# Kernel tuning notes

Hardware: AMD Instinct MI355X
Metric: run time of the kernel (lower is better)

Reference implementation:

```python
import jax, jax.numpy as jnp
import numpy as np

TAU_FILTER_INV = 1000.0
DT = 0.001
# decay = 1 - alpha = exp(-dt * tau_filter_inv)
DECAY = float(np.exp(-DT * TAU_FILTER_INV))


def setup_inputs() -> dict:
    key = jax.random.key(0)
    k1, k2, k3 = jax.random.split(key, 3)
    T, B, I, O = 2048, 32, 256, 256
    input_tensor = jax.random.normal(k1, (T, B, I), dtype=jnp.float32)
    # Linear weight init mimics uniform(-k, k), k = sqrt(1/input_size)
    k = float(np.sqrt(1.0 / I))
    W = jax.random.uniform(k2, (O, I), dtype=jnp.float32, minval=-k, maxval=k)
    b = jax.random.uniform(k3, (O,), dtype=jnp.float32, minval=-k, maxval=k)
    return {"input_tensor": input_tensor, "W": W, "b": b}


def reference(input_tensor, W, b):
    # Dense projection: [T, B, I] @ [I, O] -> [T, B, O]
    y = jnp.einsum("tbi,oi->tbo", input_tensor, W) + b
    decay = jnp.asarray(DECAY, dtype=y.dtype)

    # s(t) = y(t) + decay * s(t-1); s(0) = y(0) (init state 0)
    def step(s, x):
        s = x + decay * s
        return s, s

    _, out = jax.lax.scan(step, jnp.zeros_like(y[0]), y)
    return out
```

## Files before the change

kernel.cpp:

```cpp
#include <hip/hip_runtime.h>
#include <cstddef>


#define DECAY  0.36787944117144233f
#define D9     1.2340980408667956e-4f
#define INV1MD 1.5819767068693265f

typedef __attribute__((ext_vector_type(8))) short short8;
typedef __attribute__((ext_vector_type(4))) short short4v;
typedef __attribute__((ext_vector_type(4))) float f32x4;

static constexpr int T_DIM = 2048, B_DIM = 32, K_DIM = 256, N_DIM = 256;
static constexpr int M_DIM = T_DIM * B_DIM;
static constexpr int PS  = 32768;
static constexpr int TCH = 64;

__device__ __forceinline__ float bfbits2f(unsigned short u) {
  unsigned int x = ((unsigned int)u) << 16;
  return __builtin_bit_cast(float, x);
}
__device__ __forceinline__ short f2bf_s(float f) {
  __bf16 h = (__bf16)f;
  return __builtin_bit_cast(short, h);
}

__global__ void k_split_w(const float* __restrict__ W, short* __restrict__ Wh) {
  const int o = blockIdx.x, i = threadIdx.x;
  size_t off = (size_t)(o >> 7) * PS + (i >> 5) * 4096 + ((i >> 3) & 3) * 1024 +
               (o & 127) * 8 + (i & 7);
  Wh[off] = f2bf_s(W[o * 256 + i]);
}

__global__ __launch_bounds__(512, 6)
void k_fused(const float* __restrict__ X, const short* __restrict__ Wth,
             const float* __restrict__ bias, float* __restrict__ out) {
  __shared__ __align__(16) char ldsA[32768];
  __shared__ __align__(16) short cbh[8 * 256];
  __shared__ float cfac[TCH];

  const int tid  = threadIdx.x;
  const int lane = tid & 63;
  const int wv   = tid >> 6;
  const int c    = blockIdx.x;
  const int b    = blockIdx.y;
  const int t0   = c * TCH;
  const int ch4  = lane * 4;

  const int row16 = lane & 15;
  const int kq    = lane >> 4;
  const int cg    = wv;
  const short* Wp = Wth + (size_t)(cg >> 2) * PS;
  const int wbase = kq * 1024 + ((cg & 3) * 32 + row16) * 8;

  if (tid < TCH)
    cfac[tid] = (1.f - __expf(-(float)(t0 + tid + 1))) * INV1MD;

  f32x4 y[9];
  {
    const int ts = t0 + wv * 9 - 8;
    if (ts >= 0) {
      const float* xp = X + (size_t)ts * 8192 + b * 256 + ch4;
      #pragma unroll
      for (int j = 0; j < 9; ++j)
        y[j] = *reinterpret_cast<const f32x4*>(xp + (size_t)j * 8192);
      f32x4 s = {0.f, 0.f, 0.f, 0.f};
      #pragma unroll
      for (int j = 0; j < 9; ++j) {
        #pragma unroll
        for (int e = 0; e < 4; ++e) s[e] = fmaf(DECAY, s[e], y[j][e]);
        y[j] = s;
      }
    } else {
      y[8] = *reinterpret_cast<const f32x4*>(X + b * 256 + ch4);
    }
  }
  {
    short4v cv;
    #pragma unroll
    for (int e = 0; e < 4; ++e) cv[e] = f2bf_s(y[8][e]);
    *reinterpret_cast<short4v*>(&cbh[wv * 256 + ch4]) = cv;
  }

  short8 bh[2][2];
  #pragma unroll
  for (int ct = 0; ct < 2; ++ct)
    bh[0][ct] = *reinterpret_cast<const short8*>(Wp + wbase + ct * 128);
  __builtin_amdgcn_sched_barrier(0);

  __syncthreads();

  f32x4 cin = {0.f, 0.f, 0.f, 0.f};
  {
    float m = 1.f;
    for (int v = wv - 1; v >= 0; --v) {
      short4v cv = *reinterpret_cast<const short4v*>(&cbh[v * 256 + ch4]);
      #pragma unroll
      for (int e = 0; e < 4; ++e)
        cin[e] = fmaf(bfbits2f((unsigned short)cv[e]), m, cin[e]);
      m *= D9;
    }
  }

  {
    static constexpr float DP[9] = {
        0.36787944117144233f, 0.1353352832366127f,  0.049787068367863944f,
        0.018315638888734179f, 0.006737946999085467f, 0.0024787521766663585f,
        0.0009118819655545162f, 0.00033546262790251185f, 1.2340980408667956e-4f};
    #pragma unroll
    for (int j = 0; j < 9; ++j) {
      const int r = wv * 9 + j - 8;
      if (r >= 0) {
        short4v hv;
        #pragma unroll
        for (int e = 0; e < 4; ++e)
          hv[e] = f2bf_s(fmaf(cin[e], DP[j], y[j][e]));
        const int byte = (r * 512 + ch4 * 2) ^ ((r & 7) << 4);
        *reinterpret_cast<short4v*>(ldsA + byte) = hv;
      }
    }
  }
  __syncthreads();

  f32x4 acc[4][2] = {};
  #pragma unroll
  for (int kt = 0; kt < 8; ++kt) {
    const int cur = kt & 1;
    if (kt < 7) {
      #pragma unroll
      for (int ct = 0; ct < 2; ++ct)
        bh[cur ^ 1][ct] = *reinterpret_cast<const short8*>(
            Wp + (kt + 1) * 4096 + wbase + ct * 128);
      __builtin_amdgcn_sched_barrier(0);
    }
    #pragma unroll
    for (int rh = 0; rh < 2; ++rh) {
      short8 ah0, ah1;
      {
        const int row0 = rh * 32 + row16;
        const int b0 = (row0 * 512 + kt * 64 + kq * 16) ^ ((row0 & 7) << 4);
        const int row1 = row0 + 16;
        const int b1 = (row1 * 512 + kt * 64 + kq * 16) ^ ((row1 & 7) << 4);
        ah0 = *reinterpret_cast<const short8*>(ldsA + b0);
        ah1 = *reinterpret_cast<const short8*>(ldsA + b1);
      }
      #pragma unroll
      for (int ct = 0; ct < 2; ++ct) {
        acc[rh * 2][ct] = __builtin_amdgcn_mfma_f32_16x16x32_bf16(
            ah0, bh[cur][ct], acc[rh * 2][ct], 0, 0, 0);
        acc[rh * 2 + 1][ct] = __builtin_amdgcn_mfma_f32_16x16x32_bf16(
            ah1, bh[cur][ct], acc[rh * 2 + 1][ct], 0, 0, 0);
      }
    }
  }

  const f32x4* bias4 = reinterpret_cast<const f32x4*>(bias);
  #pragma unroll
  for (int p = 0; p < 2; ++p) {
    __syncthreads();
    #pragma unroll
    for (int rt = 2 * p; rt < 2 * p + 2; ++rt)
      #pragma unroll
      for (int ct = 0; ct < 2; ++ct)
        #pragma unroll
        for (int j = 0; j < 4; ++j) {
          const int rowh = (rt * 16 + kq * 4 + j) & 31;
          const int col  = cg * 32 + ct * 16 + row16;
          const int byte = (rowh * 1024 + col * 4) ^ ((rowh & 7) << 4);
          *reinterpret_cast<float*>(ldsA + byte) = acc[rt][ct][j];
        }
    __syncthreads();
    #pragma unroll
    for (int q = 0; q < 4; ++q) {
      const int idx  = tid + q * 512;
      const int rowh = idx >> 6;
      const int colc = idx & 63;
      const int byte = (idx * 16) ^ ((rowh & 7) << 4);
      f32x4 yv = *reinterpret_cast<const f32x4*>(ldsA + byte);
      const int row = p * 32 + rowh;
      f32x4 bv = bias4[colc];
      const float cf = cfac[row];
      f32x4 r;
      #pragma unroll
      for (int e = 0; e < 4; ++e) r[e] = fmaf(bv[e], cf, yv[e]);
      __builtin_nontemporal_store(
          r, reinterpret_cast<f32x4*>(out + ((size_t)(t0 + row) * 32 + b) * 256 +
                                      colc * 4));
    }
  }
}

__global__ void k_fb_gemm(const float* __restrict__ X, const float* __restrict__ W,
                          const float* __restrict__ bias, float* __restrict__ Y) {
  size_t idx = (size_t)blockIdx.x * 256 + threadIdx.x;
  int o = (int)(idx & 255);
  size_t m = idx >> 8;
  const float* x = X + m * 256;
  const float* w = W + (size_t)o * 256;
  float s = bias[o];
  for (int k = 0; k < 256; ++k) s = fmaf(x[k], w[k], s);
  Y[idx] = s;
}
__global__ void k_fb_scan(float* __restrict__ Y) {
  int ch = blockIdx.x * 256 + threadIdx.x;
  float s = 0.f;
  float* p = Y + ch;
  for (int t = 0; t < 2048; ++t) { s = fmaf(DECAY, s, *p); *p = s; p += 8192; }
}

extern "C" void kernel_launch(void* const* d_in, const int* in_sizes, int n_in,
                              void* d_out, int out_size, void* d_ws, size_t ws_size,
                              hipStream_t stream) {
  const float* X    = (const float*)d_in[0];
  const float* W    = (const float*)d_in[1];
  const float* bias = (const float*)d_in[2];
  float* out = (float*)d_out;

  const size_t w_elems = (size_t)N_DIM * K_DIM;
  const size_t need    = w_elems * sizeof(short);

  if (ws_size >= need) {
    short* Wh = (short*)d_ws;
    k_split_w<<<N_DIM, 256, 0, stream>>>(W, Wh);
    k_fused<<<dim3(T_DIM / TCH, B_DIM), 512, 0, stream>>>(X, Wh, bias, out);
  } else {
    k_fb_gemm<<<M_DIM, 256, 0, stream>>>(X, W, bias, out);
    k_fb_scan<<<32, 256, 0, stream>>>(out);
  }
}
```

Baseline: 34.76 us.

## Process two time chunks per block, prefetching second chunk's inputs during first GEMM

Each block now handles two consecutive 64-step time chunks instead of one, halving the grid. The X loads for the second chunk are issued before the first chunk's MFMA/epilogue phase so their latency overlaps the compute. The launch-bounds occupancy hint drops from 6 to 4 blocks per CU, which frees registers for the extra prefetched state. The cost is half as many blocks to spread over the CUs and a longer serial path inside each block.

```diff
diff --git a/kernel.cpp b/kernel.cpp
--- a/kernel.cpp
+++ b/kernel.cpp
@@ -31,7 +31,7 @@
   Wh[off] = f2bf_s(W[o * 256 + i]);
 }
 
-__global__ __launch_bounds__(512, 6)
+__global__ __launch_bounds__(512, 4)
 void k_fused(const float* __restrict__ X, const short* __restrict__ Wth,
              const float* __restrict__ bias, float* __restrict__ out) {
   __shared__ __align__(16) char ldsA[32768];
@@ -41,9 +41,9 @@
   const int tid  = threadIdx.x;
   const int lane = tid & 63;
   const int wv   = tid >> 6;
-  const int c    = blockIdx.x;
+  const int c2   = blockIdx.x;
   const int b    = blockIdx.y;
-  const int t0   = c * TCH;
+  const int t0   = c2 * 2 * TCH;
   const int ch4  = lane * 4;
 
   const int row16 = lane & 15;
@@ -52,8 +52,110 @@
   const short* Wp = Wth + (size_t)(cg >> 2) * PS;
   const int wbase = kq * 1024 + ((cg & 3) * 32 + row16) * 8;
 
-  if (tid < TCH)
-    cfac[tid] = (1.f - __expf(-(float)(t0 + tid + 1))) * INV1MD;
+  static constexpr float DP[9] = {
+      0.36787944117144233f, 0.1353352832366127f,  0.049787068367863944f,
+      0.018315638888734179f, 0.006737946999085467f, 0.0024787521766663585f,
+      0.0009118819655545162f, 0.00033546262790251185f, 1.2340980408667956e-4f};
+
+  auto publish = [&](const f32x4& s) {
+    short4v cv;
+    #pragma unroll
+    for (int e = 0; e < 4; ++e) cv[e] = f2bf_s(s[e]);
+    *reinterpret_cast<short4v*>(&cbh[wv * 256 + ch4]) = cv;
+  };
+  auto combine = [&]() {
+    f32x4 cin = {0.f, 0.f, 0.f, 0.f};
+    float m = 1.f;
+    for (int v = wv - 1; v >= 0; --v) {
+      short4v cv = *reinterpret_cast<const short4v*>(&cbh[v * 256 + ch4]);
+      #pragma unroll
+      for (int e = 0; e < 4; ++e)
+        cin[e] = fmaf(bfbits2f((unsigned short)cv[e]), m, cin[e]);
+      m *= D9;
+    }
+    return cin;
+  };
+  auto fixup = [&](f32x4 (&y)[9], const f32x4& cin) {
+    #pragma unroll
+    for (int j = 0; j < 9; ++j) {
+      const int r = wv * 9 + j - 8;
+      if (r >= 0) {
+        short4v hv;
+        #pragma unroll
+        for (int e = 0; e < 4; ++e)
+          hv[e] = f2bf_s(fmaf(cin[e], DP[j], y[j][e]));
+        const int byte = (r * 512 + ch4 * 2) ^ ((r & 7) << 4);
+        *reinterpret_cast<short4v*>(ldsA + byte) = hv;
+      }
+    }
+  };
+  auto phase_be = [&](int t0c, short8 (&bh)[2][2]) {
+    f32x4 acc[4][2] = {};
+    #pragma unroll
+    for (int kt = 0; kt < 8; ++kt) {
+      const int cur = kt & 1;
+      if (kt < 7) {
+        #pragma unroll
+        for (int ct = 0; ct < 2; ++ct)
+          bh[cur ^ 1][ct] = *reinterpret_cast<const short8*>(
+              Wp + (kt + 1) * 4096 + wbase + ct * 128);
+        __builtin_amdgcn_sched_barrier(0);
+      }
+      #pragma unroll
+      for (int rh = 0; rh < 2; ++rh) {
+        short8 ah0, ah1;
+        {
+          const int row0 = rh * 32 + row16;
+          const int b0 = (row0 * 512 + kt * 64 + kq * 16) ^ ((row0 & 7) << 4);
+          const int row1 = row0 + 16;
+          const int b1 = (row1 * 512 + kt * 64 + kq * 16) ^ ((row1 & 7) << 4);
+          ah0 = *reinterpret_cast<const short8*>(ldsA + b0);
+          ah1 = *reinterpret_cast<const short8*>(ldsA + b1);
+        }
+        #pragma unroll
+        for (int ct = 0; ct < 2; ++ct) {
+          acc[rh * 2][ct] = __builtin_amdgcn_mfma_f32_16x16x32_bf16(
+              ah0, bh[cur][ct], acc[rh * 2][ct], 0, 0, 0);
+          acc[rh * 2 + 1][ct] = __builtin_amdgcn_mfma_f32_16x16x32_bf16(
+              ah1, bh[cur][ct], acc[rh * 2 + 1][ct], 0, 0, 0);
+        }
+      }
+    }
+    const f32x4* bias4 = reinterpret_cast<const f32x4*>(bias);
+    #pragma unroll
+    for (int p = 0; p < 2; ++p) {
+      __syncthreads();
+      #pragma unroll
+      for (int rt = 2 * p; rt < 2 * p + 2; ++rt)
+        #pragma unroll
+        for (int ct = 0; ct < 2; ++ct)
+          #pragma unroll
+          for (int j = 0; j < 4; ++j) {
+            const int rowh = (rt * 16 + kq * 4 + j) & 31;
+            const int col  = cg * 32 + ct * 16 + row16;
+            const int byte = (rowh * 1024 + col * 4) ^ ((rowh & 7) << 4);
+            *reinterpret_cast<float*>(ldsA + byte) = acc[rt][ct][j];
+          }
+      __syncthreads();
+      #pragma unroll
+      for (int q = 0; q < 4; ++q) {
+        const int idx  = tid + q * 512;
+        const int rowh = idx >> 6;
+        const int colc = idx & 63;
+        const int byte = (idx * 16) ^ ((rowh & 7) << 4);
+        f32x4 yv = *reinterpret_cast<const f32x4*>(ldsA + byte);
+        const int row = p * 32 + rowh;
+        f32x4 bv = bias4[colc];
+        const float cf = cfac[row];
+        f32x4 r;
+        #pragma unroll
+        for (int e = 0; e < 4; ++e) r[e] = fmaf(bv[e], cf, yv[e]);
+        __builtin_nontemporal_store(
+            r, reinterpret_cast<f32x4*>(out +
+                   ((size_t)(t0c + row) * 32 + b) * 256 + colc * 4));
+      }
+    }
+  };
 
   f32x4 y[9];
   {
@@ -74,12 +176,7 @@
       y[8] = *reinterpret_cast<const f32x4*>(X + b * 256 + ch4);
     }
   }
-  {
-    short4v cv;
-    #pragma unroll
-    for (int e = 0; e < 4; ++e) cv[e] = f2bf_s(y[8][e]);
-    *reinterpret_cast<short4v*>(&cbh[wv * 256 + ch4]) = cv;
-  }
+  publish(y[8]);
 
   short8 bh[2][2];
   #pragma unroll
@@ -88,105 +185,52 @@
   __builtin_amdgcn_sched_barrier(0);
 
   __syncthreads();
-
-  f32x4 cin = {0.f, 0.f, 0.f, 0.f};
-  {
-    float m = 1.f;
-    for (int v = wv - 1; v >= 0; --v) {
-      short4v cv = *reinterpret_cast<const short4v*>(&cbh[v * 256 + ch4]);
-      #pragma unroll
-      for (int e = 0; e < 4; ++e)
-        cin[e] = fmaf(bfbits2f((unsigned short)cv[e]), m, cin[e]);
-      m *= D9;
-    }
-  }
-
-  {
-    static constexpr float DP[9] = {
-        0.36787944117144233f, 0.1353352832366127f,  0.049787068367863944f,
-        0.018315638888734179f, 0.006737946999085467f, 0.0024787521766663585f,
-        0.0009118819655545162f, 0.00033546262790251185f, 1.2340980408667956e-4f};
+  {
+    f32x4 cin = combine();
+    if (tid < TCH)
+      cfac[tid] = (1.f - __expf(-(float)(t0 + tid + 1))) * INV1MD;
+    fixup(y, cin);
+  }
+  __syncthreads();
+
+  f32x4 y2[9];
+  {
+    const float* xp =
+        X + (size_t)(t0 + TCH + wv * 9 - 8) * 8192 + b * 256 + ch4;
+    #pragma unroll
+    for (int j = 0; j < 9; ++j)
+      y2[j] = *reinterpret_cast<const f32x4*>(xp + (size_t)j * 8192);
+  }
+  __builtin_amdgcn_sched_barrier(0);
+
+  phase_be(t0, bh);
+
+  {
+    f32x4 s = {0.f, 0.f, 0.f, 0.f};
     #pragma unroll
     for (int j = 0; j < 9; ++j) {
-      const int r = wv * 9 + j - 8;
-      if (r >= 0) {
-        short4v hv;
-        #pragma unroll
-        for (int e = 0; e < 4; ++e)
-          hv[e] = f2bf_s(fmaf(cin[e], DP[j], y[j][e]));
-        const int byte = (r * 512 + ch4 * 2) ^ ((r & 7) << 4);
-        *reinterpret_cast<short4v*>(ldsA + byte) = hv;
-      }
-    }
-  }
-  __syncthreads();
-
-  f32x4 acc[4][2] = {};
+      #pragma unroll
+      for (int e = 0; e < 4; ++e) s[e] = fmaf(DECAY, s[e], y2[j][e]);
+      y2[j] = s;
+    }
+  }
+  publish(y2[8]);
+
   #pragma unroll
-  for (int kt = 0; kt < 8; ++kt) {
-    const int cur = kt & 1;
-    if (kt < 7) {
-      #pragma unroll
-      for (int ct = 0; ct < 2; ++ct)
-        bh[cur ^ 1][ct] = *reinterpret_cast<const short8*>(
-            Wp + (kt + 1) * 4096 + wbase + ct * 128);
-      __builtin_amdgcn_sched_barrier(0);
-    }
-    #pragma unroll
-    for (int rh = 0; rh < 2; ++rh) {
-      short8 ah0, ah1;
-      {
-        const int row0 = rh * 32 + row16;
-        const int b0 = (row0 * 512 + kt * 64 + kq * 16) ^ ((row0 & 7) << 4);
-        const int row1 = row0 + 16;
-        const int b1 = (row1 * 512 + kt * 64 + kq * 16) ^ ((row1 & 7) << 4);
-        ah0 = *reinterpret_cast<const short8*>(ldsA + b0);
-        ah1 = *reinterpret_cast<const short8*>(ldsA + b1);
-      }
-      #pragma unroll
-      for (int ct = 0; ct < 2; ++ct) {
-        acc[rh * 2][ct] = __builtin_amdgcn_mfma_f32_16x16x32_bf16(
-            ah0, bh[cur][ct], acc[rh * 2][ct], 0, 0, 0);
-        acc[rh * 2 + 1][ct] = __builtin_amdgcn_mfma_f32_16x16x32_bf16(
-            ah1, bh[cur][ct], acc[rh * 2 + 1][ct], 0, 0, 0);
-      }
-    }
-  }
-
-  const f32x4* bias4 = reinterpret_cast<const f32x4*>(bias);
-  #pragma unroll
-  for (int p = 0; p < 2; ++p) {
-    __syncthreads();
-    #pragma unroll
-    for (int rt = 2 * p; rt < 2 * p + 2; ++rt)
-      #pragma unroll
-      for (int ct = 0; ct < 2; ++ct)
-        #pragma unroll
-        for (int j = 0; j < 4; ++j) {
-          const int rowh = (rt * 16 + kq * 4 + j) & 31;
-          const int col  = cg * 32 + ct * 16 + row16;
-          const int byte = (rowh * 1024 + col * 4) ^ ((rowh & 7) << 4);
-          *reinterpret_cast<float*>(ldsA + byte) = acc[rt][ct][j];
-        }
-    __syncthreads();
-    #pragma unroll
-    for (int q = 0; q < 4; ++q) {
-      const int idx  = tid + q * 512;
-      const int rowh = idx >> 6;
-      const int colc = idx & 63;
-      const int byte = (idx * 16) ^ ((rowh & 7) << 4);
-      f32x4 yv = *reinterpret_cast<const f32x4*>(ldsA + byte);
-      const int row = p * 32 + rowh;
-      f32x4 bv = bias4[colc];
-      const float cf = cfac[row];
-      f32x4 r;
-      #pragma unroll
-      for (int e = 0; e < 4; ++e) r[e] = fmaf(bv[e], cf, yv[e]);
-      __builtin_nontemporal_store(
-          r, reinterpret_cast<f32x4*>(out + ((size_t)(t0 + row) * 32 + b) * 256 +
-                                      colc * 4));
-    }
-  }
+  for (int ct = 0; ct < 2; ++ct)
+    bh[0][ct] = *reinterpret_cast<const short8*>(Wp + wbase + ct * 128);
+  __builtin_amdgcn_sched_barrier(0);
+
+  __syncthreads();
+  {
+    f32x4 cin = combine();
+    if (tid < TCH)
+      cfac[tid] = (1.f - __expf(-(float)(t0 + TCH + tid + 1))) * INV1MD;
+    fixup(y2, cin);
+  }
+  __syncthreads();
+
+  phase_be(t0 + TCH, bh);
 }
 
 __global__ void k_fb_gemm(const float* __restrict__ X, const float* __restrict__ W,
@@ -221,7 +265,7 @@
   if (ws_size >= need) {
     short* Wh = (short*)d_ws;
     k_split_w<<<N_DIM, 256, 0, stream>>>(W, Wh);
-    k_fused<<<dim3(T_DIM / TCH, B_DIM), 512, 0, stream>>>(X, Wh, bias, out);
+    k_fused<<<dim3(T_DIM / (2 * TCH), B_DIM), 512, 0, stream>>>(X, Wh, bias, out);
   } else {
     k_fb_gemm<<<M_DIM, 256, 0, stream>>>(X, W, bias, out);
     k_fb_scan<<<32, 256, 0, stream>>>(out);
```

Result: slower. 48.18 us (+38.6%).

## Halve time chunk to 32 with 4-wave blocks and wider per-wave column tiles

Applied to the files above, without the earlier changes.

Reduces the time chunk per block from 64 to 32 and the block size from 512 to 256 threads (4 waves). Each wave now scans 10 timesteps instead of 9 and computes a 32x64 output tile instead of 64x32. The carry decay constant and the edge-case handling change to match. This doubles the grid and halves LDS per block, aiming for more parallelism and occupancy, at the cost of more blocks each doing the 8-step warm-up load and reloading W.

```diff
diff --git a/kernel.cpp b/kernel.cpp
--- a/kernel.cpp
+++ b/kernel.cpp
@@ -3,7 +3,7 @@
 
 
 #define DECAY  0.36787944117144233f
-#define D9     1.2340980408667956e-4f
+#define D10    4.5399929762484854e-5f
 #define INV1MD 1.5819767068693265f
 
 typedef __attribute__((ext_vector_type(8))) short short8;
@@ -13,7 +13,7 @@
 static constexpr int T_DIM = 2048, B_DIM = 32, K_DIM = 256, N_DIM = 256;
 static constexpr int M_DIM = T_DIM * B_DIM;
 static constexpr int PS  = 32768;
-static constexpr int TCH = 64;
+static constexpr int TCH = 32;
 
 __device__ __forceinline__ float bfbits2f(unsigned short u) {
   unsigned int x = ((unsigned int)u) << 16;
@@ -31,11 +31,11 @@
   Wh[off] = f2bf_s(W[o * 256 + i]);
 }
 
-__global__ __launch_bounds__(512, 6)
+__global__ __launch_bounds__(256, 5)
 void k_fused(const float* __restrict__ X, const short* __restrict__ Wth,
              const float* __restrict__ bias, float* __restrict__ out) {
-  __shared__ __align__(16) char ldsA[32768];
-  __shared__ __align__(16) short cbh[8 * 256];
+  __shared__ __align__(16) char ldsA[16384];
+  __shared__ __align__(16) short cbh[4 * 256];
   __shared__ float cfac[TCH];
 
   const int tid  = threadIdx.x;
@@ -49,41 +49,45 @@
   const int row16 = lane & 15;
   const int kq    = lane >> 4;
   const int cg    = wv;
-  const short* Wp = Wth + (size_t)(cg >> 2) * PS;
-  const int wbase = kq * 1024 + ((cg & 3) * 32 + row16) * 8;
+  const short* Wp = Wth + (size_t)(cg >> 1) * PS;
+  const int wbase = kq * 1024 + ((cg & 1) * 64 + row16) * 8;
 
   if (tid < TCH)
     cfac[tid] = (1.f - __expf(-(float)(t0 + tid + 1))) * INV1MD;
 
-  f32x4 y[9];
-  {
-    const int ts = t0 + wv * 9 - 8;
+  f32x4 y[10];
+  {
+    const int ts = t0 + wv * 10 - 8;
     if (ts >= 0) {
       const float* xp = X + (size_t)ts * 8192 + b * 256 + ch4;
       #pragma unroll
-      for (int j = 0; j < 9; ++j)
+      for (int j = 0; j < 10; ++j)
         y[j] = *reinterpret_cast<const f32x4*>(xp + (size_t)j * 8192);
       f32x4 s = {0.f, 0.f, 0.f, 0.f};
       #pragma unroll
-      for (int j = 0; j < 9; ++j) {
+      for (int j = 0; j < 10; ++j) {
         #pragma unroll
         for (int e = 0; e < 4; ++e) s[e] = fmaf(DECAY, s[e], y[j][e]);
         y[j] = s;
       }
     } else {
-      y[8] = *reinterpret_cast<const f32x4*>(X + b * 256 + ch4);
+      f32x4 x0 = *reinterpret_cast<const f32x4*>(X + b * 256 + ch4);
+      f32x4 x1 = *reinterpret_cast<const f32x4*>(X + 8192 + b * 256 + ch4);
+      y[8] = x0;
+      #pragma unroll
+      for (int e = 0; e < 4; ++e) y[9][e] = fmaf(DECAY, x0[e], x1[e]);
     }
   }
   {
     short4v cv;
     #pragma unroll
-    for (int e = 0; e < 4; ++e) cv[e] = f2bf_s(y[8][e]);
+    for (int e = 0; e < 4; ++e) cv[e] = f2bf_s(y[9][e]);
     *reinterpret_cast<short4v*>(&cbh[wv * 256 + ch4]) = cv;
   }
 
-  short8 bh[2][2];
+  short8 bh[2][4];
   #pragma unroll
-  for (int ct = 0; ct < 2; ++ct)
+  for (int ct = 0; ct < 4; ++ct)
     bh[0][ct] = *reinterpret_cast<const short8*>(Wp + wbase + ct * 128);
   __builtin_amdgcn_sched_barrier(0);
 
@@ -97,18 +101,19 @@
       #pragma unroll
       for (int e = 0; e < 4; ++e)
         cin[e] = fmaf(bfbits2f((unsigned short)cv[e]), m, cin[e]);
-      m *= D9;
-    }
-  }
-
-  {
-    static constexpr float DP[9] = {
-        0.36787944117144233f, 0.1353352832366127f,  0.049787068367863944f,
+      m *= D10;
+    }
+  }
+
+  {
+    static constexpr float DP[10] = {
+        0.36787944117144233f,  0.1353352832366127f,   0.049787068367863944f,
         0.018315638888734179f, 0.006737946999085467f, 0.0024787521766663585f,
-        0.0009118819655545162f, 0.00033546262790251185f, 1.2340980408667956e-4f};
-    #pragma unroll
-    for (int j = 0; j < 9; ++j) {
-      const int r = wv * 9 + j - 8;
+        0.0009118819655545162f, 0.00033546262790251185f,
+        1.2340980408667956e-4f, 4.5399929762484854e-5f};
+    #pragma unroll
+    for (int j = 0; j < 10; ++j) {
+      const int r = wv * 10 + j - 8;
       if (r >= 0) {
         short4v hv;
         #pragma unroll
@@ -121,35 +126,31 @@
   }
   __syncthreads();
 
-  f32x4 acc[4][2] = {};
+  f32x4 acc[2][4] = {};
   #pragma unroll
   for (int kt = 0; kt < 8; ++kt) {
     const int cur = kt & 1;
     if (kt < 7) {
       #pragma unroll
-      for (int ct = 0; ct < 2; ++ct)
+      for (int ct = 0; ct < 4; ++ct)
         bh[cur ^ 1][ct] = *reinterpret_cast<const short8*>(
             Wp + (kt + 1) * 4096 + wbase + ct * 128);
       __builtin_amdgcn_sched_barrier(0);
     }
-    #pragma unroll
-    for (int rh = 0; rh < 2; ++rh) {
-      short8 ah0, ah1;
-      {
-        const int row0 = rh * 32 + row16;
-        const int b0 = (row0 * 512 + kt * 64 + kq * 16) ^ ((row0 & 7) << 4);
-        const int row1 = row0 + 16;
-        const int b1 = (row1 * 512 + kt * 64 + kq * 16) ^ ((row1 & 7) << 4);
-        ah0 = *reinterpret_cast<const short8*>(ldsA + b0);
-        ah1 = *reinterpret_cast<const short8*>(ldsA + b1);
-      }
-      #pragma unroll
-      for (int ct = 0; ct < 2; ++ct) {
-        acc[rh * 2][ct] = __builtin_amdgcn_mfma_f32_16x16x32_bf16(
-            ah0, bh[cur][ct], acc[rh * 2][ct], 0, 0, 0);
-        acc[rh * 2 + 1][ct] = __builtin_amdgcn_mfma_f32_16x16x32_bf16(
-            ah1, bh[cur][ct], acc[rh * 2 + 1][ct], 0, 0, 0);
-      }
+    short8 ah0, ah1;
+    {
+      const int b0 = (row16 * 512 + kt * 64 + kq * 16) ^ ((row16 & 7) << 4);
+      const int row1 = row16 + 16;
+      const int b1 = (row1 * 512 + kt * 64 + kq * 16) ^ ((row1 & 7) << 4);
+      ah0 = *reinterpret_cast<const short8*>(ldsA + b0);
+      ah1 = *reinterpret_cast<const short8*>(ldsA + b1);
+    }
+    #pragma unroll
+    for (int ct = 0; ct < 4; ++ct) {
+      acc[0][ct] = __builtin_amdgcn_mfma_f32_16x16x32_bf16(
+          ah0, bh[cur][ct], acc[0][ct], 0, 0, 0);
+      acc[1][ct] = __builtin_amdgcn_mfma_f32_16x16x32_bf16(
+          ah1, bh[cur][ct], acc[1][ct], 0, 0, 0);
     }
   }
 
@@ -158,25 +159,23 @@
   for (int p = 0; p < 2; ++p) {
     __syncthreads();
     #pragma unroll
-    for (int rt = 2 * p; rt < 2 * p + 2; ++rt)
-      #pragma unroll
-      for (int ct = 0; ct < 2; ++ct)
-        #pragma unroll
-        for (int j = 0; j < 4; ++j) {
-          const int rowh = (rt * 16 + kq * 4 + j) & 31;
-          const int col  = cg * 32 + ct * 16 + row16;
-          const int byte = (rowh * 1024 + col * 4) ^ ((rowh & 7) << 4);
-          *reinterpret_cast<float*>(ldsA + byte) = acc[rt][ct][j];
-        }
+    for (int ct = 0; ct < 4; ++ct)
+      #pragma unroll
+      for (int j = 0; j < 4; ++j) {
+        const int rowh = kq * 4 + j;
+        const int col  = cg * 64 + ct * 16 + row16;
+        const int byte = (rowh * 1024 + col * 4) ^ ((rowh & 7) << 4);
+        *reinterpret_cast<float*>(ldsA + byte) = acc[p][ct][j];
+      }
     __syncthreads();
     #pragma unroll
     for (int q = 0; q < 4; ++q) {
-      const int idx  = tid + q * 512;
+      const int idx  = tid + q * 256;
       const int rowh = idx >> 6;
       const int colc = idx & 63;
       const int byte = (idx * 16) ^ ((rowh & 7) << 4);
       f32x4 yv = *reinterpret_cast<const f32x4*>(ldsA + byte);
-      const int row = p * 32 + rowh;
+      const int row = p * 16 + rowh;
       f32x4 bv = bias4[colc];
       const float cf = cfac[row];
       f32x4 r;
@@ -221,7 +220,7 @@
   if (ws_size >= need) {
     short* Wh = (short*)d_ws;
     k_split_w<<<N_DIM, 256, 0, stream>>>(W, Wh);
-    k_fused<<<dim3(T_DIM / TCH, B_DIM), 512, 0, stream>>>(X, Wh, bias, out);
+    k_fused<<<dim3(T_DIM / TCH, B_DIM), 256, 0, stream>>>(X, Wh, bias, out);
   } else {
     k_fb_gemm<<<M_DIM, 256, 0, stream>>>(X, W, bias, out);
     k_fb_scan<<<32, 256, 0, stream>>>(out);
```

New measurement: 39.24 us. 1.13x slower.
